# Kernel tuning notes

Hardware: AMD Instinct MI355X
Metric: run time of the kernel (lower is better)

The kernel has to match this reference:

```python
import jax, jax.numpy as jnp
import numpy as np

B, S, H = 128, 1024, 256
NEG = 1e9

def setup_inputs() -> dict:
    key = jax.random.key(0)
    ks = jax.random.split(key, 11)
    sc = 0.05
    return {
        'ref': jax.random.normal(ks[0], (B, S, H), jnp.float32),
        'query': jax.random.normal(ks[1], (B, H), jnp.float32),
        'mask': jax.random.randint(ks[2], (B, S), 0, 2, jnp.int32),
        'wg': jax.random.normal(ks[3], (H, H), jnp.float32) * sc,
        'bg': jax.random.normal(ks[4], (H,), jnp.float32) * sc,
        'wqg': jax.random.normal(ks[5], (H, H), jnp.float32) * sc,
        'vg': jax.random.normal(ks[6], (H,), jnp.float32) * sc,
        'wp': jax.random.normal(ks[7], (H, H), jnp.float32) * sc,
        'bp': jax.random.normal(ks[8], (H,), jnp.float32) * sc,
        'wqp': jax.random.normal(ks[9], (H, H), jnp.float32) * sc,
        'vp': jax.random.normal(ks[10], (H,), jnp.float32) * sc,
    }

def reference(ref, query, mask, wg, bg, wqg, vg, wp, bp, wqp, vp):
    # Bahdanau additive pointer attention with glimpse, per PointerDecoder.pointer_net
    maskf = mask.astype(ref.dtype)
    # glimpse attention
    enc_g = jnp.einsum('bsd,hd->bsh', ref, wg) + bg            # conv1d kernel=1
    q_g = jnp.einsum('bd,hd->bh', query, wqg)                   # w_q_g (no bias)
    scores_g = jnp.einsum('bsh,h->bs', jnp.tanh(enc_g + q_g[:, None, :]), vg)
    att_g = jax.nn.softmax(scores_g - maskf * NEG, axis=-1)     # [B,S]
    glimpse = jnp.einsum('bs,bsd->bd', att_g, ref) + query      # [B,H]
    # pointer scores
    enc_p = jnp.einsum('bsd,hd->bsh', ref, wp) + bp
    q_p = jnp.einsum('bd,hd->bh', glimpse, wqp)
    scores_p = jnp.einsum('bsh,h->bs', jnp.tanh(enc_p + q_p[:, None, :]), vp)
    masked_scores = scores_p - maskf * NEG                      # [B,S]
    return masked_scores
```

## Files before the change

kernel.cpp:

```cpp
#include <hip/hip_runtime.h>

#define Bb 128
#define Ss 1024
#define Hh 256
#define NEGF 1e9f

typedef short bf16x8 __attribute__((ext_vector_type(8)));
typedef float f32x4 __attribute__((ext_vector_type(4)));

__device__ __forceinline__ short f2bf(float f) {
    union { float f; unsigned u; } c; c.f = f;
    return (short)((c.u + 0x8000u) >> 16);
}

__device__ __forceinline__ bf16x8 ld_bf8_f32(const float* p) {
    const float4* p4 = (const float4*)p;
    float4 a = p4[0], b = p4[1];
    bf16x8 r;
    r[0] = f2bf(a.x); r[1] = f2bf(a.y); r[2] = f2bf(a.z); r[3] = f2bf(a.w);
    r[4] = f2bf(b.x); r[5] = f2bf(b.y); r[6] = f2bf(b.z); r[7] = f2bf(b.w);
    return r;
}

__device__ __forceinline__ float fast_tanh(float x) {
    float cl = fminf(fmaxf(x, -10.f), 10.f);
    float e = __expf(2.f * cl);
    return (e - 1.f) * __builtin_amdgcn_rcpf(e + 1.f);
}

__device__ __forceinline__ void stage16(const short* g, short* l) {
    __builtin_amdgcn_global_load_lds((const __attribute__((address_space(1))) void*)g,
                                     (__attribute__((address_space(3))) void*)l, 16, 0, 0);
}

__global__ __launch_bounds__(256) void convert_w(const float* __restrict__ wg,
                                                 const float* __restrict__ wp,
                                                 short* __restrict__ wgb,
                                                 short* __restrict__ wpb) {
    int i = blockIdx.x * 256 + threadIdx.x;
    wgb[i] = f2bf(wg[i]);
    wpb[i] = f2bf(wp[i]);
}

__global__ __launch_bounds__(256) void dot_qb(const float* __restrict__ q,
                                              const float* __restrict__ W,
                                              const float* __restrict__ bias,
                                              float* __restrict__ out) {
    int b = blockIdx.x, h = threadIdx.x;
    const float4* qr = (const float4*)(q + b * Hh);
    const float4* wr = (const float4*)(W + h * Hh);
    float acc = 0.f;
#pragma unroll 8
    for (int i = 0; i < Hh / 4; ++i) {
        float4 q4 = qr[i], w4 = wr[i];
        acc += q4.x * w4.x + q4.y * w4.y + q4.z * w4.z + q4.w * w4.w;
    }
    out[b * Hh + h] = acc + bias[h];
}

template <int MASKED>
__global__ __launch_bounds__(256) void scores_mfma(const float* __restrict__ ref,
                                                   const short* __restrict__ Wbf,
                                                   const float* __restrict__ qbias,
                                                   const float* __restrict__ vvec,
                                                   const int* __restrict__ mask,
                                                   float* __restrict__ out) {
    __shared__ short Wlds[2][4096];
    const int b = blockIdx.x;
    const int s0 = blockIdx.y * 128;
    const int t = threadIdx.x;
    const int wave = t >> 6;
    const int lane = t & 63;
    const int nl = lane & 15;
    const int quad = lane >> 4;
    const int rowbase = s0 + wave * 32;

    const int soff0 = (t & 15) * Hh + (t >> 6) * 32 + ((t >> 4) & 3) * 8;
    const int soff1 = soff0 + 128;
    const int dbase0 = wave * 512;
    const int dbase1 = 2048 + wave * 512;

    bf16x8 afrag[2][8];
#pragma unroll
    for (int rt = 0; rt < 2; ++rt) {
        const float* rp = ref + ((size_t)b * Ss + rowbase + rt * 16 + nl) * Hh;
#pragma unroll
        for (int kb = 0; kb < 8; ++kb)
            afrag[rt][kb] = ld_bf8_f32(rp + kb * 32 + quad * 8);
    }

    stage16(Wbf + soff0, &Wlds[0][dbase0]);
    stage16(Wbf + soff1, &Wlds[0][dbase1]);
    __syncthreads();

    float sc[2][4] = {{0.f, 0.f, 0.f, 0.f}, {0.f, 0.f, 0.f, 0.f}};

    for (int nc = 0; nc < 16; ++nc) {
        const int cur = nc & 1;
        if (nc < 15) {
            const short* gsrc = Wbf + ((nc + 1) << 12);
            stage16(gsrc + soff0, &Wlds[1 - cur][dbase0]);
            stage16(gsrc + soff1, &Wlds[1 - cur][dbase1]);
        }
        const int n = nc * 16 + nl;
        const float qb = qbias[b * Hh + n];
        const float vv = vvec[n];
        bf16x8 bfrag[8];
#pragma unroll
        for (int kb = 0; kb < 8; ++kb)
            bfrag[kb] = *(const bf16x8*)&Wlds[cur][kb * 512 + lane * 8];
#pragma unroll
        for (int rt = 0; rt < 2; ++rt) {
            f32x4 c = {0.f, 0.f, 0.f, 0.f};
#pragma unroll
            for (int kb = 0; kb < 8; ++kb)
                c = __builtin_amdgcn_mfma_f32_16x16x32_bf16(afrag[rt][kb], bfrag[kb], c, 0, 0, 0);
#pragma unroll
            for (int r = 0; r < 4; ++r)
                sc[rt][r] += fast_tanh(c[r] + qb) * vv;
        }
        __syncthreads();
    }

#pragma unroll
    for (int rt = 0; rt < 2; ++rt)
#pragma unroll
        for (int r = 0; r < 4; ++r) {
            float v = sc[rt][r];
            v += __shfl_xor(v, 1, 64);
            v += __shfl_xor(v, 2, 64);
            v += __shfl_xor(v, 4, 64);
            v += __shfl_xor(v, 8, 64);
            sc[rt][r] = v;
        }

    if (nl == 0) {
#pragma unroll
        for (int rt = 0; rt < 2; ++rt)
#pragma unroll
            for (int r = 0; r < 4; ++r) {
                int m = rowbase + rt * 16 + quad * 4 + r;
                float v = sc[rt][r];
                if (MASKED) v -= (float)mask[b * Ss + m] * NEGF;
                out[(size_t)b * Ss + m] = v;
            }
    }
}

__global__ __launch_bounds__(1024) void softmax_kernel(const float* __restrict__ scores,
                                                       const int* __restrict__ mask,
                                                       float* __restrict__ att) {
    int b = blockIdx.x, t = threadIdx.x;
    __shared__ float red[16];
    int idx = b * Ss + t;
    float x = scores[idx] - (float)mask[idx] * NEGF;

    float m = x;
#pragma unroll
    for (int o = 1; o < 64; o <<= 1) m = fmaxf(m, __shfl_xor(m, o, 64));
    if ((t & 63) == 0) red[t >> 6] = m;
    __syncthreads();
    float M = red[0];
#pragma unroll
    for (int j = 1; j < 16; ++j) M = fmaxf(M, red[j]);
    __syncthreads();

    float e = __expf(x - M);
    float s = e;
#pragma unroll
    for (int o = 1; o < 64; o <<= 1) s += __shfl_xor(s, o, 64);
    if ((t & 63) == 0) red[t >> 6] = s;
    __syncthreads();
    float S = 0.f;
#pragma unroll
    for (int j = 0; j < 16; ++j) S += red[j];

    att[idx] = e * __builtin_amdgcn_rcpf(S);
}

__global__ __launch_bounds__(256) void glimpse_part(const float* __restrict__ ref,
                                                    const float* __restrict__ att,
                                                    float* __restrict__ gpart) {
    int b = blockIdx.x, q = blockIdx.y, d = threadIdx.x;
    const float* rp = ref + ((size_t)b * Ss + q * 128) * Hh + d;
    const float* ap = att + b * Ss + q * 128;
    float acc = 0.f;
#pragma unroll 8
    for (int s = 0; s < 128; ++s) acc += ap[s] * rp[(size_t)s * Hh];
    gpart[(b * 8 + q) * Hh + d] = acc;
}

__global__ __launch_bounds__(256) void qbias_p_kernel(const float* __restrict__ gpart,
                                                      const float* __restrict__ query,
                                                      const float* __restrict__ wqp,
                                                      const float* __restrict__ bp,
                                                      float* __restrict__ out) {
    int b = blockIdx.x, t = threadIdx.x;
    __shared__ __align__(16) float gl[Hh];
    float g = query[b * Hh + t];
#pragma unroll
    for (int q = 0; q < 8; ++q) g += gpart[(b * 8 + q) * Hh + t];
    gl[t] = g;
    __syncthreads();
    const float4* wr = (const float4*)(wqp + t * Hh);
    const float4* gp = (const float4*)gl;
    float acc = 0.f;
#pragma unroll 8
    for (int i = 0; i < Hh / 4; ++i) {
        float4 w4 = wr[i];
        float4 g4 = gp[i];
        acc += w4.x * g4.x + w4.y * g4.y + w4.z * g4.z + w4.w * g4.w;
    }
    out[b * Hh + t] = acc + bp[t];
}

extern "C" void kernel_launch(void* const* d_in, const int* in_sizes, int n_in,
                              void* d_out, int out_size, void* d_ws, size_t ws_size,
                              hipStream_t stream) {
    const float* ref   = (const float*)d_in[0];
    const float* query = (const float*)d_in[1];
    const int*   mask  = (const int*)d_in[2];
    const float* wg    = (const float*)d_in[3];
    const float* bg    = (const float*)d_in[4];
    const float* wqg   = (const float*)d_in[5];
    const float* vg    = (const float*)d_in[6];
    const float* wp    = (const float*)d_in[7];
    const float* bp    = (const float*)d_in[8];
    const float* wqp   = (const float*)d_in[9];
    const float* vp    = (const float*)d_in[10];
    float* out = (float*)d_out;

    char* ws = (char*)d_ws;
    short* wg_bf    = (short*)(ws + 0);
    short* wp_bf    = (short*)(ws + 131072);
    float* qbias_g  = (float*)(ws + 262144);
    float* qbias_p  = (float*)(ws + 393216);
    float* scores_g = (float*)(ws + 524288);
    float* att      = (float*)(ws + 1048576);
    float* gpart    = (float*)(ws + 1572864);

    convert_w<<<Hh * Hh / 256, 256, 0, stream>>>(wg, wp, wg_bf, wp_bf);
    dot_qb<<<Bb, Hh, 0, stream>>>(query, wqg, bg, qbias_g);
    scores_mfma<0><<<dim3(Bb, Ss / 128), 256, 0, stream>>>(ref, wg_bf, qbias_g, vg, nullptr, scores_g);
    softmax_kernel<<<Bb, Ss, 0, stream>>>(scores_g, mask, att);
    glimpse_part<<<dim3(Bb, 8), 256, 0, stream>>>(ref, att, gpart);
    qbias_p_kernel<<<Bb, Hh, 0, stream>>>(gpart, query, wqp, bp, qbias_p);
    scores_mfma<1><<<dim3(Bb, Ss / 128), 256, 0, stream>>>(ref, wp_bf, qbias_p, vp, mask, out);
}
```

Measured before the change: 313.2 us.

## Pre-convert ref to bf16 once and reuse across scoring and glimpse kernels

New measurement: 313.4 us. No clear change (+0.1%).

```diff
diff --git a/kernel.cpp b/kernel.cpp
--- a/kernel.cpp
+++ b/kernel.cpp
@@ -13,13 +13,18 @@
     return (short)((c.u + 0x8000u) >> 16);
 }
 
-__device__ __forceinline__ bf16x8 ld_bf8_f32(const float* p) {
-    const float4* p4 = (const float4*)p;
-    float4 a = p4[0], b = p4[1];
-    bf16x8 r;
-    r[0] = f2bf(a.x); r[1] = f2bf(a.y); r[2] = f2bf(a.z); r[3] = f2bf(a.w);
-    r[4] = f2bf(b.x); r[5] = f2bf(b.y); r[6] = f2bf(b.z); r[7] = f2bf(b.w);
-    return r;
+__device__ __forceinline__ unsigned pack2bf(float lo, float hi) {
+    union { float f; unsigned u; } a, b; a.f = lo; b.f = hi;
+    unsigned al = (a.u + 0x8000u) >> 16;
+    unsigned bh = (b.u + 0x8000u) & 0xFFFF0000u;
+    return al | bh;
+}
+
+__device__ __forceinline__ float bfhi2f(unsigned u) {
+    union { unsigned u; float f; } c; c.u = u & 0xFFFF0000u; return c.f;
+}
+__device__ __forceinline__ float bflo2f(unsigned u) {
+    union { unsigned u; float f; } c; c.u = u << 16; return c.f;
 }
 
 __device__ __forceinline__ float fast_tanh(float x) {
@@ -31,6 +36,19 @@
 __device__ __forceinline__ void stage16(const short* g, short* l) {
     __builtin_amdgcn_global_load_lds((const __attribute__((address_space(1))) void*)g,
                                      (__attribute__((address_space(3))) void*)l, 16, 0, 0);
+}
+
+__global__ __launch_bounds__(256) void convert_ref(const float* __restrict__ ref,
+                                                   uint4* __restrict__ refb) {
+    size_t i = (size_t)blockIdx.x * 256 + threadIdx.x;
+    const float4* p = (const float4*)ref + i * 2;
+    float4 a = p[0], b = p[1];
+    uint4 o;
+    o.x = pack2bf(a.x, a.y);
+    o.y = pack2bf(a.z, a.w);
+    o.z = pack2bf(b.x, b.y);
+    o.w = pack2bf(b.z, b.w);
+    refb[i] = o;
 }
 
 __global__ __launch_bounds__(256) void convert_w(const float* __restrict__ wg,
@@ -59,13 +77,13 @@
 }
 
 template <int MASKED>
-__global__ __launch_bounds__(256) void scores_mfma(const float* __restrict__ ref,
+__global__ __launch_bounds__(256) void scores_mfma(const short* __restrict__ refb,
                                                    const short* __restrict__ Wbf,
                                                    const float* __restrict__ qbias,
                                                    const float* __restrict__ vvec,
                                                    const int* __restrict__ mask,
                                                    float* __restrict__ out) {
-    __shared__ short Wlds[2][4096];
+    __shared__ short Wlds[2][8192];
     const int b = blockIdx.x;
     const int s0 = blockIdx.y * 128;
     const int t = threadIdx.x;
@@ -83,41 +101,48 @@
     bf16x8 afrag[2][8];
 #pragma unroll
     for (int rt = 0; rt < 2; ++rt) {
-        const float* rp = ref + ((size_t)b * Ss + rowbase + rt * 16 + nl) * Hh;
+        const short* rp = refb + ((size_t)b * Ss + rowbase + rt * 16 + nl) * Hh;
 #pragma unroll
         for (int kb = 0; kb < 8; ++kb)
-            afrag[rt][kb] = ld_bf8_f32(rp + kb * 32 + quad * 8);
+            afrag[rt][kb] = *(const bf16x8*)(rp + kb * 32 + quad * 8);
     }
 
     stage16(Wbf + soff0, &Wlds[0][dbase0]);
     stage16(Wbf + soff1, &Wlds[0][dbase1]);
+    stage16(Wbf + 16 * Hh + soff0, &Wlds[0][4096 + dbase0]);
+    stage16(Wbf + 16 * Hh + soff1, &Wlds[0][4096 + dbase1]);
     __syncthreads();
 
     float sc[2][4] = {{0.f, 0.f, 0.f, 0.f}, {0.f, 0.f, 0.f, 0.f}};
 
-    for (int nc = 0; nc < 16; ++nc) {
-        const int cur = nc & 1;
-        if (nc < 15) {
-            const short* gsrc = Wbf + ((nc + 1) << 12);
-            stage16(gsrc + soff0, &Wlds[1 - cur][dbase0]);
-            stage16(gsrc + soff1, &Wlds[1 - cur][dbase1]);
+    for (int nc2 = 0; nc2 < 8; ++nc2) {
+        const int cur = nc2 & 1;
+        if (nc2 < 7) {
+            const short* g = Wbf + (size_t)(nc2 + 1) * 32 * Hh;
+            stage16(g + soff0, &Wlds[1 - cur][dbase0]);
+            stage16(g + soff1, &Wlds[1 - cur][dbase1]);
+            stage16(g + 16 * Hh + soff0, &Wlds[1 - cur][4096 + dbase0]);
+            stage16(g + 16 * Hh + soff1, &Wlds[1 - cur][4096 + dbase1]);
         }
-        const int n = nc * 16 + nl;
-        const float qb = qbias[b * Hh + n];
-        const float vv = vvec[n];
-        bf16x8 bfrag[8];
-#pragma unroll
-        for (int kb = 0; kb < 8; ++kb)
-            bfrag[kb] = *(const bf16x8*)&Wlds[cur][kb * 512 + lane * 8];
-#pragma unroll
-        for (int rt = 0; rt < 2; ++rt) {
-            f32x4 c = {0.f, 0.f, 0.f, 0.f};
+#pragma unroll
+        for (int h = 0; h < 2; ++h) {
+            const int n = nc2 * 32 + h * 16 + nl;
+            const float qb = qbias[b * Hh + n];
+            const float vv = vvec[n];
+            bf16x8 bfrag[8];
 #pragma unroll
             for (int kb = 0; kb < 8; ++kb)
-                c = __builtin_amdgcn_mfma_f32_16x16x32_bf16(afrag[rt][kb], bfrag[kb], c, 0, 0, 0);
-#pragma unroll
-            for (int r = 0; r < 4; ++r)
-                sc[rt][r] += fast_tanh(c[r] + qb) * vv;
+                bfrag[kb] = *(const bf16x8*)&Wlds[cur][h * 4096 + kb * 512 + lane * 8];
+#pragma unroll
+            for (int rt = 0; rt < 2; ++rt) {
+                f32x4 c = {0.f, 0.f, 0.f, 0.f};
+#pragma unroll
+                for (int kb = 0; kb < 8; ++kb)
+                    c = __builtin_amdgcn_mfma_f32_16x16x32_bf16(afrag[rt][kb], bfrag[kb], c, 0, 0, 0);
+#pragma unroll
+                for (int r = 0; r < 4; ++r)
+                    sc[rt][r] += fast_tanh(c[r] + qb) * vv;
+            }
         }
         __syncthreads();
     }
@@ -178,16 +203,34 @@
     att[idx] = e * __builtin_amdgcn_rcpf(S);
 }
 
-__global__ __launch_bounds__(256) void glimpse_part(const float* __restrict__ ref,
+__global__ __launch_bounds__(256) void glimpse_part(const unsigned* __restrict__ refb,
                                                     const float* __restrict__ att,
                                                     float* __restrict__ gpart) {
-    int b = blockIdx.x, q = blockIdx.y, d = threadIdx.x;
-    const float* rp = ref + ((size_t)b * Ss + q * 128) * Hh + d;
+    int b = blockIdx.x, q = blockIdx.y, t = threadIdx.x;
+    const int c = t & 31;
+    const int rg = t >> 5;
+    __shared__ float part[8][Hh];
+    const unsigned* base = refb + ((size_t)(b * Ss + q * 128)) * (Hh / 2);
     const float* ap = att + b * Ss + q * 128;
-    float acc = 0.f;
-#pragma unroll 8
-    for (int s = 0; s < 128; ++s) acc += ap[s] * rp[(size_t)s * Hh];
-    gpart[(b * 8 + q) * Hh + d] = acc;
+
+    float acc[8] = {0.f, 0.f, 0.f, 0.f, 0.f, 0.f, 0.f, 0.f};
+#pragma unroll 4
+    for (int it = 0; it < 16; ++it) {
+        int row = it * 8 + rg;
+        float a = ap[row];
+        uint4 v = *(const uint4*)(base + (size_t)row * (Hh / 2) + c * 4);
+        acc[0] += a * bflo2f(v.x); acc[1] += a * bfhi2f(v.x);
+        acc[2] += a * bflo2f(v.y); acc[3] += a * bfhi2f(v.y);
+        acc[4] += a * bflo2f(v.z); acc[5] += a * bfhi2f(v.z);
+        acc[6] += a * bflo2f(v.w); acc[7] += a * bfhi2f(v.w);
+    }
+#pragma unroll
+    for (int j = 0; j < 8; ++j) part[rg][c * 8 + j] = acc[j];
+    __syncthreads();
+    float s = 0.f;
+#pragma unroll
+    for (int g = 0; g < 8; ++g) s += part[g][t];
+    gpart[(size_t)(b * 8 + q) * Hh + t] = s;
 }
 
 __global__ __launch_bounds__(256) void qbias_p_kernel(const float* __restrict__ gpart,
@@ -231,19 +274,22 @@
     float* out = (float*)d_out;
 
     char* ws = (char*)d_ws;
-    short* wg_bf    = (short*)(ws + 0);
-    short* wp_bf    = (short*)(ws + 131072);
-    float* qbias_g  = (float*)(ws + 262144);
-    float* qbias_p  = (float*)(ws + 393216);
-    float* scores_g = (float*)(ws + 524288);
-    float* att      = (float*)(ws + 1048576);
-    float* gpart    = (float*)(ws + 1572864);
-
+    short* ref_bf   = (short*)(ws + 0);
+    size_t off = (size_t)Bb * Ss * Hh * 2;
+    short* wg_bf    = (short*)(ws + off);               off += 131072;
+    short* wp_bf    = (short*)(ws + off);               off += 131072;
+    float* qbias_g  = (float*)(ws + off);               off += 131072;
+    float* qbias_p  = (float*)(ws + off);               off += 131072;
+    float* scores_g = (float*)(ws + off);               off += 524288;
+    float* att      = (float*)(ws + off);               off += 524288;
+    float* gpart    = (float*)(ws + off);
+
+    convert_ref<<<(Bb * Ss * Hh) / 2048, 256, 0, stream>>>(ref, (uint4*)ref_bf);
     convert_w<<<Hh * Hh / 256, 256, 0, stream>>>(wg, wp, wg_bf, wp_bf);
     dot_qb<<<Bb, Hh, 0, stream>>>(query, wqg, bg, qbias_g);
-    scores_mfma<0><<<dim3(Bb, Ss / 128), 256, 0, stream>>>(ref, wg_bf, qbias_g, vg, nullptr, scores_g);
+    scores_mfma<0><<<dim3(Bb, Ss / 128), 256, 0, stream>>>(ref_bf, wg_bf, qbias_g, vg, nullptr, scores_g);
     softmax_kernel<<<Bb, Ss, 0, stream>>>(scores_g, mask, att);
-    glimpse_part<<<dim3(Bb, 8), 256, 0, stream>>>(ref, att, gpart);
+    glimpse_part<<<dim3(Bb, 8), 256, 0, stream>>>((const unsigned*)ref_bf, att, gpart);
     qbias_p_kernel<<<Bb, Hh, 0, stream>>>(gpart, query, wqp, bp, qbias_p);
-    scores_mfma<1><<<dim3(Bb, Ss / 128), 256, 0, stream>>>(ref, wp_bf, qbias_p, vp, mask, out);
-}
+    scores_mfma<1><<<dim3(Bb, Ss / 128), 256, 0, stream>>>(ref_bf, wp_bf, qbias_p, vp, mask, out);
+}
```
